# Kernel tuning notes

Measured on AMD Instinct MI355X. Metric: run time of the kernel, lower is better.

Reference implementation:

```python
import jax, jax.numpy as jnp
import numpy as np

N0, N1, N2 = 100000, 50000, 25000
E0, E1 = 400000, 200000
H1, D1 = 4, 64   # layer0: 4 heads x 64
H2, D2 = 1, 64   # layer1: 1 head  x 64
SLOPE = 0.2      # DGL GATConv leaky_relu negative_slope


def gat_conv(h_src, h_dst, src, dst, W, attn_l, attn_r, bias, n_dst, heads, d):
    # linear projection (shared between src and dst, as in DGL GATConv)
    f_src = (h_src @ W).reshape(-1, heads, d)   # (N_src, H, D)
    f_dst = (h_dst @ W).reshape(-1, heads, d)   # (N_dst, H, D)
    el = jnp.einsum('nhd,hd->nh', f_src, attn_l)  # (N_src, H)
    er = jnp.einsum('nhd,hd->nh', f_dst, attn_r)  # (N_dst, H)
    e = jax.nn.leaky_relu(el[src] + er[dst], SLOPE)  # (E, H)
    # edge-softmax over incoming edges of each dst node (numerically stable)
    m = jax.ops.segment_max(e, dst, num_segments=n_dst)      # (N_dst, H)
    ee = jnp.exp(e - m[dst])
    s = jax.ops.segment_sum(ee, dst, num_segments=n_dst)
    alpha = ee / s[dst]                                      # (E, H)
    msg = f_src[src] * alpha[:, :, None]                     # (E, H, D)
    out = jax.ops.segment_sum(msg, dst, num_segments=n_dst)  # (N_dst, H, D)
    return out + bias.reshape(1, heads, d)


def setup_inputs() -> dict:
    key = jax.random.key(0)
    ks = jax.random.split(key, 12)
    return {
        'x': jax.random.normal(ks[0], (N0, 256), jnp.float32),
        'e0_src': jax.random.randint(ks[1], (E0,), 0, N0, jnp.int32),
        'e0_dst': jax.random.randint(ks[2], (E0,), 0, N1, jnp.int32),
        'e1_src': jax.random.randint(ks[3], (E1,), 0, N1, jnp.int32),
        'e1_dst': jax.random.randint(ks[4], (E1,), 0, N2, jnp.int32),
        'W1': jax.random.normal(ks[5], (256, H1 * D1), jnp.float32) * 0.06,
        'al1': jax.random.normal(ks[6], (H1, D1), jnp.float32) * 0.1,
        'ar1': jax.random.normal(ks[7], (H1, D1), jnp.float32) * 0.1,
        'b1': jnp.zeros((H1 * D1,), jnp.float32),
        'W2': jax.random.normal(ks[8], (H1 * D1, H2 * D2), jnp.float32) * 0.06,
        'al2': jax.random.normal(ks[9], (H2, D2), jnp.float32) * 0.1,
        'ar2': jax.random.normal(ks[10], (H2, D2), jnp.float32) * 0.1,
        'b2': jnp.zeros((H2 * D2,), jnp.float32),
    }


def reference(x, e0_src, e0_dst, e1_src, e1_dst,
              W1, al1, ar1, b1, W2, al2, ar2, b2):
    # layer 0: block 100k src -> 50k dst; dst nodes are a prefix of src nodes
    h = gat_conv(x, x[:N1], e0_src, e0_dst, W1, al1, ar1, b1, N1, H1, D1)
    h = jax.nn.relu(h).reshape(N1, H1 * D1)   # activation + flatten(1); dropout is identity at eval
    # layer 1 (final): single head, no activation, flatten
    h = gat_conv(h, h[:N2], e1_src, e1_dst, W2, al2, ar2, b2, N2, H2, D2)
    return h.reshape(N2, H2 * D2)
```

## Files before the change

kernel.cpp:

```cpp
#include <hip/hip_runtime.h>
#include <cstddef>
#include <cstdint>

constexpr int cN0 = 100000, cN1 = 50000, cN2 = 25000;
constexpr int cE0 = 400000, cE1 = 200000;
constexpr float SLOPE = 0.2f;

typedef short short8  __attribute__((ext_vector_type(8)));
typedef float f32x4   __attribute__((ext_vector_type(4)));

__device__ __forceinline__ unsigned short f2bf(float x) {
    union { float f; uint32_t u; } c; c.f = x;
    uint32_t u = c.u + 0x7FFFu + ((c.u >> 16) & 1u);
    return (unsigned short)(u >> 16);
}
__device__ __forceinline__ float bf2f(uint32_t u) {
    union { uint32_t u; float f; } c; c.u = u << 16; return c.f;
}
__device__ __forceinline__ float lrelu(float x) { return x >= 0.f ? x : SLOPE * x; }

__device__ __forceinline__ uint32_t cvtpk(float lo, float hi) {
    uint32_t r;
    asm("v_cvt_pk_bf16_f32 %0, %1, %2" : "=v"(r) : "v"(lo), "v"(hi));
    return r;
}

__device__ __forceinline__ void gload_lds16(const void* g, void* l) {
    __builtin_amdgcn_global_load_lds(
        (const __attribute__((address_space(1))) unsigned int*)g,
        (__attribute__((address_space(3))) unsigned int*)l, 16, 0, 0);
}


__global__ void hist2_kernel(const int* __restrict__ d0, const int* __restrict__ d1,
                             int* __restrict__ cnt0, int* __restrict__ cnt1) {
    int i = blockIdx.x * blockDim.x + threadIdx.x;
    if (i < cE0) atomicAdd(&cnt0[d0[i]], 1);
    int j = i - cE0;
    if (j >= 0 && j < cE1) atomicAdd(&cnt1[d1[j]], 1);
}

__global__ __launch_bounds__(256) void chunk_sum2_kernel(const int* __restrict__ cnt0, int n0,
                                                         const int* __restrict__ cnt1, int n1,
                                                         int* __restrict__ bsum0, int* __restrict__ bsum1,
                                                         int nblk1) {
    const int* cnt = blockIdx.y ? cnt1 : cnt0;
    int n = blockIdx.y ? n1 : n0;
    int* bsum = blockIdx.y ? bsum1 : bsum0;
    if (blockIdx.y && (int)blockIdx.x >= nblk1) return;
    int i = blockIdx.x * 256 + threadIdx.x;
    int v = (i < n) ? cnt[i] : 0;
    #pragma unroll
    for (int o = 32; o; o >>= 1) v += __shfl_xor(v, o);
    __shared__ int ws[4];
    if ((threadIdx.x & 63) == 0) ws[threadIdx.x >> 6] = v;
    __syncthreads();
    if (threadIdx.x == 0) bsum[blockIdx.x] = ws[0] + ws[1] + ws[2] + ws[3];
}

__device__ __forceinline__ int block_exscan(int v, int& total) {
    int lane = threadIdx.x & 63, w = threadIdx.x >> 6;
    int x = v;
    #pragma unroll
    for (int o = 1; o < 64; o <<= 1) { int t = __shfl_up(x, o); if (lane >= o) x += t; }
    __shared__ int ws[4];
    if (lane == 63) ws[w] = x;
    __syncthreads();
    int add = 0;
    #pragma unroll
    for (int i = 0; i < 4; ++i) if (i < w) add += ws[i];
    total = ws[0] + ws[1] + ws[2] + ws[3];
    return add + x - v;
}

__global__ __launch_bounds__(256) void top_scan2_kernel(const int* __restrict__ bsum0, int nblk0,
                                                        const int* __restrict__ bsum1, int nblk1,
                                                        int* __restrict__ boff0, int* __restrict__ boff1,
                                                        int* __restrict__ tot0, int* __restrict__ tot1) {
    int i = threadIdx.x;
    int tot;
    int v = (i < nblk0) ? bsum0[i] : 0;
    int e = block_exscan(v, tot);
    if (i < nblk0) boff0[i] = e;
    if (i == 0) *tot0 = tot;
    __syncthreads();
    v = (i < nblk1) ? bsum1[i] : 0;
    e = block_exscan(v, tot);
    if (i < nblk1) boff1[i] = e;
    if (i == 0) *tot1 = tot;
}

__global__ __launch_bounds__(256) void chunk_scan2_kernel(const int* __restrict__ cnt0, int n0,
                                                          const int* __restrict__ cnt1, int n1,
                                                          const int* __restrict__ boff0, const int* __restrict__ boff1,
                                                          int* __restrict__ offs0, int* __restrict__ cursor0,
                                                          int* __restrict__ offs1, int* __restrict__ cursor1,
                                                          int nblk1) {
    const int* cnt = blockIdx.y ? cnt1 : cnt0;
    const int* boff = blockIdx.y ? boff1 : boff0;
    int* offs = blockIdx.y ? offs1 : offs0;
    int* cursor = blockIdx.y ? cursor1 : cursor0;
    int n = blockIdx.y ? n1 : n0;
    if (blockIdx.y && (int)blockIdx.x >= nblk1) return;
    int i = blockIdx.x * 256 + threadIdx.x;
    int v = (i < n) ? cnt[i] : 0;
    int tot; int e = block_exscan(v, tot) + boff[blockIdx.x];
    if (i < n) { offs[i] = e; cursor[i] = e; }
}

__global__ void scatter2_kernel(const int* __restrict__ s0, const int* __restrict__ d0,
                                const int* __restrict__ s1, const int* __restrict__ d1,
                                int* __restrict__ cursor0, int* __restrict__ srcidx0,
                                int* __restrict__ cursor1, int* __restrict__ srcidx1) {
    int i = blockIdx.x * blockDim.x + threadIdx.x;
    if (i < cE0) { int p = atomicAdd(&cursor0[d0[i]], 1); srcidx0[p] = s0[i]; }
    int j = i - cE0;
    if (j >= 0 && j < cE1) { int p = atomicAdd(&cursor1[d1[j]], 1); srcidx1[p] = s1[j]; }
}

__global__ __launch_bounds__(256) void bf16_transpose2_kernel(const float* __restrict__ W1,
                                                              const float* __restrict__ W2,
                                                              short* __restrict__ bt1,
                                                              short* __restrict__ bt2) {
    int i = blockIdx.x * 256 + threadIdx.x;
    if (i < 256 * 256) {
        int k = i >> 8, n = i & 255;
        bt1[(size_t)n * 256 + k] = (short)f2bf(W1[i]);
    } else {
        int j = i - 256 * 256;
        if (j < 256 * 64) {
            int k = j >> 6, n = j & 63;
            bt2[(size_t)n * 256 + k] = (short)f2bf(W2[j]);
        }
    }
}

__global__ __launch_bounds__(512, 4) void gemm0_deep(
    const float* __restrict__ A, const short* __restrict__ BT,
    unsigned short* __restrict__ C,
    const float* __restrict__ al, const float* __restrict__ ar,
    float* __restrict__ el, float* __restrict__ er,
    int M, int erN)
{
    constexpr int T = 8;
    constexpr int nh = 4;
    __shared__ float Asm[2][128 * 32];
    __shared__ short Bsm[2][256 * 32];

    const int tid = threadIdx.x;
    const int w = tid >> 6;
    const int lane = tid & 63;
    const int ln = lane & 15;
    const int kg = lane >> 4;
    const int wr = w >> 2;
    const int wc = w & 3;
    const int m0 = blockIdx.x * 128;

    f32x4 acc[4][4];
    #pragma unroll
    for (int mi = 0; mi < 4; ++mi)
        #pragma unroll
        for (int ni = 0; ni < 4; ++ni)
            #pragma unroll
            for (int j = 0; j < 4; ++j) acc[mi][ni][j] = 0.f;

    auto stageA = [&](int k0, int b) {
        #pragma unroll
        for (int q = 0; q < 2; ++q) {
            int ci = w + q * 8;
            int r = ci * 8 + (lane >> 3);
            int cl = (lane & 7) ^ (r & 7);
            int gr = m0 + r; if (gr >= M) gr = M - 1;
            gload_lds16(&A[(size_t)gr * 256 + k0 + cl * 4], &Asm[b][ci * 256]);
        }
    };
    auto stageB = [&](int k0, int b) {
        #pragma unroll
        for (int q = 0; q < 2; ++q) {
            int ci = w + q * 8;
            int r = ci * 16 + (lane >> 2);
            int cl = (lane & 3) ^ ((r >> 1) & 3);
            gload_lds16(&BT[(size_t)r * 256 + k0 + cl * 8], &Bsm[b][ci * 512]);
        }
    };

    stageA(0, 0); stageB(0, 0);
    __syncthreads();

    const int swa = ln & 7;
    const int p0base = 2 * kg;
    const int pb = kg ^ ((ln >> 1) & 3);

    int cur = 0;
    #pragma unroll
    for (int t = 0; t < T; ++t) {
        if (t + 1 < T) { stageA((t + 1) * 32, cur ^ 1); stageB((t + 1) * 32, cur ^ 1); }

        short8 af[4];
        {
            int pA = p0base ^ swa;
            #pragma unroll
            for (int mi = 0; mi < 4; ++mi) {
                int r = wr * 64 + mi * 16 + ln;
                const f32x4 q0 = *(const f32x4*)&Asm[cur][r * 32 + pA * 4];
                const f32x4 q1 = *(const f32x4*)&Asm[cur][r * 32 + (pA ^ 1) * 4];
                union { uint32_t u[4]; short8 s; } cv;
                cv.u[0] = cvtpk(q0[0], q0[1]);
                cv.u[1] = cvtpk(q0[2], q0[3]);
                cv.u[2] = cvtpk(q1[0], q1[1]);
                cv.u[3] = cvtpk(q1[2], q1[3]);
                af[mi] = cv.s;
            }
        }
        #pragma unroll
        for (int ni = 0; ni < 4; ++ni) {
            int rB = wc * 64 + ni * 16 + ln;
            short8 bf = *(const short8*)&Bsm[cur][rB * 32 + pb * 8];
            #pragma unroll
            for (int mi = 0; mi < 4; ++mi)
                acc[mi][ni] = __builtin_amdgcn_mfma_f32_16x16x32_bf16(af[mi], bf, acc[mi][ni], 0, 0, 0);
        }
        __syncthreads();
        cur ^= 1;
    }

    const int h = wc;
    float alv[4], arv[4];
    #pragma unroll
    for (int ni = 0; ni < 4; ++ni) {
        alv[ni] = al[h * 64 + ni * 16 + ln];
        arv[ni] = ar[h * 64 + ni * 16 + ln];
    }
    #pragma unroll
    for (int mi = 0; mi < 4; ++mi) {
        float pl[4] = {0, 0, 0, 0}, pr[4] = {0, 0, 0, 0};
        #pragma unroll
        for (int ni = 0; ni < 4; ++ni)
            #pragma unroll
            for (int j = 0; j < 4; ++j) {
                float v = acc[mi][ni][j];
                pl[j] += v * alv[ni];
                pr[j] += v * arv[ni];
            }
        #pragma unroll
        for (int j = 0; j < 4; ++j)
            #pragma unroll
            for (int o = 1; o < 16; o <<= 1) {
                pl[j] += __shfl_xor(pl[j], o);
                pr[j] += __shfl_xor(pr[j], o);
            }
        #pragma unroll
        for (int j = 0; j < 4; ++j) {
            int row = m0 + wr * 64 + mi * 16 + kg * 4 + j;
            if (row < M) {
                #pragma unroll
                for (int ni = 0; ni < 4; ++ni)
                    C[(size_t)row * 256 + wc * 64 + ni * 16 + ln] = f2bf(acc[mi][ni][j]);
                if (ln == 0) {
                    el[row * nh + h] = pl[j];
                    if (row < erN) er[row * nh + h] = pr[j];
                }
            }
        }
    }
}

__global__ __launch_bounds__(1024) void agg0_fused(
    const int* __restrict__ offs, const int* __restrict__ srcidx,
    const float* __restrict__ el, const float* __restrict__ er,
    const unsigned short* __restrict__ fb, const float* __restrict__ bias,
    const short* __restrict__ bt2,
    const float* __restrict__ al2, const float* __restrict__ ar2,
    unsigned short* __restrict__ f2b, float* __restrict__ el2, float* __restrict__ er2)
{
    constexpr int PITCH = 264;
    __shared__ short Bs2[64 * 256];
    __shared__ short h1s[16 * PITCH];
    __shared__ float partE[4][16];
    __shared__ float partR[4][16];

    const int tid = threadIdx.x;
    const int w = tid >> 6;
    const int lane = tid & 63;
    const int n = blockIdx.x * 16 + w;

    #pragma unroll
    for (int i = 0; i < 2; ++i) {
        int seg = 2 * (i * 16 + w);
        int r = seg + (lane >> 5);
        int c = (lane & 31) ^ (r & 7);
        gload_lds16(&bt2[(size_t)r * 256 + c * 8], &Bs2[(size_t)seg * 256]);
    }

    int beg = offs[n], end = offs[n + 1];

    int h4 = lane & 3, sub = lane >> 2;
    float erA = er[n * 4 + h4];
    float m = -1e30f, s = 0.f;
    for (int i = beg + sub; i < end; i += 16) {
        int sv = srcidx[i];
        float e = lrelu(el[sv * 4 + h4] + erA);
        if (e > m) { s = s * __expf(m - e) + 1.f; m = e; }
        else s += __expf(e - m);
    }
    #pragma unroll
    for (int o = 4; o < 64; o <<= 1) {
        float m2 = __shfl_xor(m, o), s2 = __shfl_xor(s, o);
        float M = fmaxf(m, m2);
        s = s * __expf(m - M) + s2 * __expf(m2 - M);
        m = M;
    }
    float inv = (s > 0.f) ? 1.f / s : 0.f;

    int q = lane >> 4, lcol = lane & 15;
    int hB = lcol >> 2;
    float mB = __shfl(m, hB);
    float invB = __shfl(inv, hB);
    float erB = __shfl(erA, hB);

    float a[16] = {};
    for (int i = beg + q; i < end; i += 4) {
        int sv = srcidx[i];
        float e = lrelu(el[sv * 4 + hB] + erB);
        float p = __expf(e - mB) * invB;
        const uint4* rp = (const uint4*)&fb[(size_t)sv * 256 + lcol * 16];
        uint4 v0 = rp[0];
        uint4 v1 = rp[1];
        a[0]  = fmaf(bf2f(v0.x & 0xffffu), p, a[0]);
        a[1]  = fmaf(bf2f(v0.x >> 16),     p, a[1]);
        a[2]  = fmaf(bf2f(v0.y & 0xffffu), p, a[2]);
        a[3]  = fmaf(bf2f(v0.y >> 16),     p, a[3]);
        a[4]  = fmaf(bf2f(v0.z & 0xffffu), p, a[4]);
        a[5]  = fmaf(bf2f(v0.z >> 16),     p, a[5]);
        a[6]  = fmaf(bf2f(v0.w & 0xffffu), p, a[6]);
        a[7]  = fmaf(bf2f(v0.w >> 16),     p, a[7]);
        a[8]  = fmaf(bf2f(v1.x & 0xffffu), p, a[8]);
        a[9]  = fmaf(bf2f(v1.x >> 16),     p, a[9]);
        a[10] = fmaf(bf2f(v1.y & 0xffffu), p, a[10]);
        a[11] = fmaf(bf2f(v1.y >> 16),     p, a[11]);
        a[12] = fmaf(bf2f(v1.z & 0xffffu), p, a[12]);
        a[13] = fmaf(bf2f(v1.z >> 16),     p, a[13]);
        a[14] = fmaf(bf2f(v1.w & 0xffffu), p, a[14]);
        a[15] = fmaf(bf2f(v1.w >> 16),     p, a[15]);
    }
    #pragma unroll
    for (int j = 0; j < 16; ++j) {
        a[j] += __shfl_xor(a[j], 16);
        a[j] += __shfl_xor(a[j], 32);
    }

    if (lane < 16) {
        float4 b0 = *(const float4*)&bias[lane * 16 + 0];
        float4 b1 = *(const float4*)&bias[lane * 16 + 4];
        float4 b2 = *(const float4*)&bias[lane * 16 + 8];
        float4 b3 = *(const float4*)&bias[lane * 16 + 12];
        float bb[16] = { b0.x, b0.y, b0.z, b0.w, b1.x, b1.y, b1.z, b1.w,
                         b2.x, b2.y, b2.z, b2.w, b3.x, b3.y, b3.z, b3.w };
        short8 r0, r1;
        #pragma unroll
        for (int j = 0; j < 8; ++j) {
            float o = a[j] + bb[j];
            r0[j] = (short)f2bf(o > 0.f ? o : 0.f);
        }
        #pragma unroll
        for (int j = 0; j < 8; ++j) {
            float o = a[8 + j] + bb[8 + j];
            r1[j] = (short)f2bf(o > 0.f ? o : 0.f);
        }
        *(short8*)&h1s[w * PITCH + lane * 16] = r0;
        *(short8*)&h1s[w * PITCH + lane * 16 + 8] = r1;
    }
    __syncthreads();

    if (w < 4) {
        const int ln = lane & 15, kg = lane >> 4;
        const int cc = w * 16 + ln;
        f32x4 acc2;
        #pragma unroll
        for (int j = 0; j < 4; ++j) acc2[j] = 0.f;
        #pragma unroll
        for (int kt = 0; kt < 8; ++kt) {
            short8 af = *(const short8*)&h1s[ln * PITCH + kt * 32 + kg * 8];
            short8 bf = *(const short8*)&Bs2[cc * 256 + ((kt * 4 + kg) ^ (cc & 7)) * 8];
            acc2 = __builtin_amdgcn_mfma_f32_16x16x32_bf16(af, bf, acc2, 0, 0, 0);
        }
        float alc = al2[cc], arc = ar2[cc];
        #pragma unroll
        for (int j = 0; j < 4; ++j) {
            int node = kg * 4 + j;
            float v = acc2[j];
            f2b[((size_t)(blockIdx.x * 16 + node)) * 64 + cc] = f2bf(v);
            float pe = v * alc, pr = v * arc;
            #pragma unroll
            for (int o = 1; o < 16; o <<= 1) {
                pe += __shfl_xor(pe, o);
                pr += __shfl_xor(pr, o);
            }
            if (ln == 0) { partE[w][node] = pe; partR[w][node] = pr; }
        }
    }
    __syncthreads();
    if (tid < 16) {
        int gn = blockIdx.x * 16 + tid;
        float e = partE[0][tid] + partE[1][tid] + partE[2][tid] + partE[3][tid];
        el2[gn] = e;
        if (gn < cN2) {
            float r = partR[0][tid] + partR[1][tid] + partR[2][tid] + partR[3][tid];
            er2[gn] = r;
        }
    }
}

__global__ __launch_bounds__(256) void agg1_kernel(const int* __restrict__ offs,
                                                   const int* __restrict__ srcidx,
                                                   const float* __restrict__ el,
                                                   const float* __restrict__ er,
                                                   const unsigned short* __restrict__ f2b,
                                                   const float* __restrict__ bias,
                                                   float* __restrict__ out) {
    int w = threadIdx.x >> 6, lane = threadIdx.x & 63;
    int n = blockIdx.x * 4 + w;
    if (n >= cN2) return;
    int beg = offs[n], end = offs[n + 1];
    float ern = er[n];

    float m = -1e30f, s = 0.f;
    for (int i = beg + lane; i < end; i += 64) {
        float e = lrelu(el[srcidx[i]] + ern);
        if (e > m) { s = s * __expf(m - e) + 1.f; m = e; }
        else s += __expf(e - m);
    }
    #pragma unroll
    for (int o = 1; o < 64; o <<= 1) {
        float m2 = __shfl_xor(m, o), s2 = __shfl_xor(s, o);
        float M = fmaxf(m, m2);
        s = s * __expf(m - M) + s2 * __expf(m2 - M);
        m = M;
    }
    float inv = (s > 0.f) ? 1.f / s : 0.f;

    int q = lane >> 3, lcol = lane & 7;
    float a[8] = {};
    for (int i = beg + q; i < end; i += 8) {
        int sv = srcidx[i];
        float e = lrelu(el[sv] + ern);
        float p = __expf(e - m) * inv;
        uint4 v = *(const uint4*)&f2b[(size_t)sv * 64 + lcol * 8];
        a[0] = fmaf(bf2f(v.x & 0xffffu), p, a[0]);
        a[1] = fmaf(bf2f(v.x >> 16),     p, a[1]);
        a[2] = fmaf(bf2f(v.y & 0xffffu), p, a[2]);
        a[3] = fmaf(bf2f(v.y >> 16),     p, a[3]);
        a[4] = fmaf(bf2f(v.z & 0xffffu), p, a[4]);
        a[5] = fmaf(bf2f(v.z >> 16),     p, a[5]);
        a[6] = fmaf(bf2f(v.w & 0xffffu), p, a[6]);
        a[7] = fmaf(bf2f(v.w >> 16),     p, a[7]);
    }
    #pragma unroll
    for (int j = 0; j < 8; ++j) {
        a[j] += __shfl_xor(a[j], 8);
        a[j] += __shfl_xor(a[j], 16);
        a[j] += __shfl_xor(a[j], 32);
    }
    if (q == 0) {
        float4 o0, o1;
        o0.x = a[0] + bias[lcol * 8 + 0];
        o0.y = a[1] + bias[lcol * 8 + 1];
        o0.z = a[2] + bias[lcol * 8 + 2];
        o0.w = a[3] + bias[lcol * 8 + 3];
        o1.x = a[4] + bias[lcol * 8 + 4];
        o1.y = a[5] + bias[lcol * 8 + 5];
        o1.z = a[6] + bias[lcol * 8 + 6];
        o1.w = a[7] + bias[lcol * 8 + 7];
        *(float4*)&out[(size_t)n * 64 + lcol * 8] = o0;
        *(float4*)&out[(size_t)n * 64 + lcol * 8 + 4] = o1;
    }
}


extern "C" void kernel_launch(void* const* d_in, const int* in_sizes, int n_in,
                              void* d_out, int out_size, void* d_ws, size_t ws_size,
                              hipStream_t stream) {
    const float* x      = (const float*)d_in[0];
    const int*   e0_src = (const int*)d_in[1];
    const int*   e0_dst = (const int*)d_in[2];
    const int*   e1_src = (const int*)d_in[3];
    const int*   e1_dst = (const int*)d_in[4];
    const float* W1     = (const float*)d_in[5];
    const float* al1    = (const float*)d_in[6];
    const float* ar1    = (const float*)d_in[7];
    const float* b1     = (const float*)d_in[8];
    const float* W2     = (const float*)d_in[9];
    const float* al2    = (const float*)d_in[10];
    const float* ar2    = (const float*)d_in[11];
    const float* b2     = (const float*)d_in[12];
    float* out = (float*)d_out;

    char* ws = (char*)d_ws;
    size_t off = 0;
    auto alloc = [&](size_t bytes) -> void* {
        void* p = ws + off;
        off = (off + bytes + 255) & ~(size_t)255;
        return p;
    };
    unsigned short* fb  = (unsigned short*)alloc((size_t)cN0 * 256 * 2);
    unsigned short* f2b = (unsigned short*)alloc((size_t)cN1 * 64 * 2);
    float* el0  = (float*)alloc((size_t)cN0 * 4 * 4);
    float* er0  = (float*)alloc((size_t)cN1 * 4 * 4);
    float* el2  = (float*)alloc((size_t)cN1 * 4);
    float* er2  = (float*)alloc((size_t)cN2 * 4);
    short* bt1  = (short*)alloc((size_t)256 * 256 * 2);
    short* bt2  = (short*)alloc((size_t)64 * 256 * 2);
    int* cntB    = (int*)alloc((size_t)(cN1 + cN2) * 4);
    int* cnt0    = cntB;
    int* cnt1    = cntB + cN1;
    int* offs0   = (int*)alloc((size_t)(cN1 + 1) * 4);
    int* cursor0 = (int*)alloc((size_t)cN1 * 4);
    int* srcidx0 = (int*)alloc((size_t)cE0 * 4);
    int* offs1   = (int*)alloc((size_t)(cN2 + 1) * 4);
    int* cursor1 = (int*)alloc((size_t)cN2 * 4);
    int* srcidx1 = (int*)alloc((size_t)cE1 * 4);
    int* bsum0   = (int*)alloc(256 * 4);
    int* boff0   = (int*)alloc(256 * 4);
    int* bsum1   = (int*)alloc(256 * 4);
    int* boff1   = (int*)alloc(256 * 4);
    (void)ws_size; (void)n_in; (void)in_sizes; (void)out_size;

    const int nblk0 = (cN1 + 255) / 256;
    const int nblk1 = (cN2 + 255) / 256;

    hipMemsetAsync(cntB, 0, (size_t)(cN1 + cN2) * 4, stream);
    hist2_kernel<<<(cE0 + cE1 + 255) / 256, 256, 0, stream>>>(e0_dst, e1_dst, cnt0, cnt1);
    chunk_sum2_kernel<<<dim3(nblk0, 2), 256, 0, stream>>>(cnt0, cN1, cnt1, cN2, bsum0, bsum1, nblk1);
    top_scan2_kernel<<<1, 256, 0, stream>>>(bsum0, nblk0, bsum1, nblk1, boff0, boff1,
                                            offs0 + cN1, offs1 + cN2);
    chunk_scan2_kernel<<<dim3(nblk0, 2), 256, 0, stream>>>(cnt0, cN1, cnt1, cN2, boff0, boff1,
                                                           offs0, cursor0, offs1, cursor1, nblk1);
    scatter2_kernel<<<(cE0 + cE1 + 255) / 256, 256, 0, stream>>>(e0_src, e0_dst, e1_src, e1_dst,
                                                                 cursor0, srcidx0, cursor1, srcidx1);
    bf16_transpose2_kernel<<<(256 * 256 + 256 * 64 + 255) / 256, 256, 0, stream>>>(W1, W2, bt1, bt2);

    gemm0_deep<<<(cN0 + 127) / 128, 512, 0, stream>>>(x, bt1, fb, al1, ar1, el0, er0, cN0, cN1);

    agg0_fused<<<cN1 / 16, 1024, 0, stream>>>(offs0, srcidx0, el0, er0, fb, b1,
                                              bt2, al2, ar2, f2b, el2, er2);

    agg1_kernel<<<(cN2 + 3) / 4, 256, 0, stream>>>(offs1, srcidx1, el2, er2, f2b, b2, out);
}
```

Measured before the change: 188.2 us.

## Replace 16-node MFMA fused layer-1 projection with per-wave scalar dot products

Shrinks the layer-0 aggregation kernel from 1024-thread blocks handling 16 nodes to 256-thread blocks handling 4 nodes. Each wave now computes its own node's 64-wide layer-1 projection with scalar bf16 FMAs, reading W2 rows straight from global memory instead of staging them in LDS and using MFMA. This removes the large LDS footprint and both block-wide barriers, which should raise occupancy and cut sync cost. In exchange, every wave re-reads the full 32KB W2 matrix through the cache hierarchy and does the projection on plain ALUs rather than matrix cores.

```diff
diff --git a/kernel.cpp b/kernel.cpp
--- a/kernel.cpp
+++ b/kernel.cpp
@@ -265,7 +265,7 @@
     }
 }
 
-__global__ __launch_bounds__(1024) void agg0_fused(
+__global__ __launch_bounds__(256) void agg0_kernel(
     const int* __restrict__ offs, const int* __restrict__ srcidx,
     const float* __restrict__ el, const float* __restrict__ er,
     const unsigned short* __restrict__ fb, const float* __restrict__ bias,
@@ -273,25 +273,11 @@
     const float* __restrict__ al2, const float* __restrict__ ar2,
     unsigned short* __restrict__ f2b, float* __restrict__ el2, float* __restrict__ er2)
 {
-    constexpr int PITCH = 264;
-    __shared__ short Bs2[64 * 256];
-    __shared__ short h1s[16 * PITCH];
-    __shared__ float partE[4][16];
-    __shared__ float partR[4][16];
-
-    const int tid = threadIdx.x;
-    const int w = tid >> 6;
-    const int lane = tid & 63;
-    const int n = blockIdx.x * 16 + w;
-
-    #pragma unroll
-    for (int i = 0; i < 2; ++i) {
-        int seg = 2 * (i * 16 + w);
-        int r = seg + (lane >> 5);
-        int c = (lane & 31) ^ (r & 7);
-        gload_lds16(&bt2[(size_t)r * 256 + c * 8], &Bs2[(size_t)seg * 256]);
-    }
-
+    __shared__ short h1s[4][256];
+
+    int w = threadIdx.x >> 6, lane = threadIdx.x & 63;
+    int n = blockIdx.x * 4 + w;
+    if (n >= cN1) return;
     int beg = offs[n], end = offs[n + 1];
 
     int h4 = lane & 3, sub = lane >> 2;
@@ -349,65 +335,44 @@
         a[j] += __shfl_xor(a[j], 32);
     }
 
-    if (lane < 16) {
-        float4 b0 = *(const float4*)&bias[lane * 16 + 0];
-        float4 b1 = *(const float4*)&bias[lane * 16 + 4];
-        float4 b2 = *(const float4*)&bias[lane * 16 + 8];
-        float4 b3 = *(const float4*)&bias[lane * 16 + 12];
-        float bb[16] = { b0.x, b0.y, b0.z, b0.w, b1.x, b1.y, b1.z, b1.w,
-                         b2.x, b2.y, b2.z, b2.w, b3.x, b3.y, b3.z, b3.w };
+    if (q == 0) {
         short8 r0, r1;
         #pragma unroll
         for (int j = 0; j < 8; ++j) {
-            float o = a[j] + bb[j];
+            float o = a[j] + bias[lcol * 16 + j];
             r0[j] = (short)f2bf(o > 0.f ? o : 0.f);
         }
         #pragma unroll
         for (int j = 0; j < 8; ++j) {
-            float o = a[8 + j] + bb[8 + j];
+            float o = a[8 + j] + bias[lcol * 16 + 8 + j];
             r1[j] = (short)f2bf(o > 0.f ? o : 0.f);
         }
-        *(short8*)&h1s[w * PITCH + lane * 16] = r0;
-        *(short8*)&h1s[w * PITCH + lane * 16 + 8] = r1;
-    }
-    __syncthreads();
-
-    if (w < 4) {
-        const int ln = lane & 15, kg = lane >> 4;
-        const int cc = w * 16 + ln;
-        f32x4 acc2;
-        #pragma unroll
-        for (int j = 0; j < 4; ++j) acc2[j] = 0.f;
-        #pragma unroll
-        for (int kt = 0; kt < 8; ++kt) {
-            short8 af = *(const short8*)&h1s[ln * PITCH + kt * 32 + kg * 8];
-            short8 bf = *(const short8*)&Bs2[cc * 256 + ((kt * 4 + kg) ^ (cc & 7)) * 8];
-            acc2 = __builtin_amdgcn_mfma_f32_16x16x32_bf16(af, bf, acc2, 0, 0, 0);
-        }
-        float alc = al2[cc], arc = ar2[cc];
-        #pragma unroll
-        for (int j = 0; j < 4; ++j) {
-            int node = kg * 4 + j;
-            float v = acc2[j];
-            f2b[((size_t)(blockIdx.x * 16 + node)) * 64 + cc] = f2bf(v);
-            float pe = v * alc, pr = v * arc;
-            #pragma unroll
-            for (int o = 1; o < 16; o <<= 1) {
-                pe += __shfl_xor(pe, o);
-                pr += __shfl_xor(pr, o);
-            }
-            if (ln == 0) { partE[w][node] = pe; partR[w][node] = pr; }
-        }
-    }
-    __syncthreads();
-    if (tid < 16) {
-        int gn = blockIdx.x * 16 + tid;
-        float e = partE[0][tid] + partE[1][tid] + partE[2][tid] + partE[3][tid];
-        el2[gn] = e;
-        if (gn < cN2) {
-            float r = partR[0][tid] + partR[1][tid] + partR[2][tid] + partR[3][tid];
-            er2[gn] = r;
-        }
+        *(short8*)&h1s[w][lcol * 16] = r0;
+        *(short8*)&h1s[w][lcol * 16 + 8] = r1;
+    }
+
+    float acc2 = 0.f;
+    const short* wrow = &bt2[(size_t)lane * 256];
+    #pragma unroll 8
+    for (int kt = 0; kt < 32; ++kt) {
+        short8 hv = *(const short8*)&h1s[w][kt * 8];
+        short8 wv = *(const short8*)&wrow[kt * 8];
+        #pragma unroll
+        for (int j = 0; j < 8; ++j)
+            acc2 = fmaf(bf2f((uint32_t)(unsigned short)hv[j]),
+                        bf2f((uint32_t)(unsigned short)wv[j]), acc2);
+    }
+    f2b[(size_t)n * 64 + lane] = f2bf(acc2);
+    float pe = acc2 * al2[lane];
+    float pr = acc2 * ar2[lane];
+    #pragma unroll
+    for (int o = 1; o < 64; o <<= 1) {
+        pe += __shfl_xor(pe, o);
+        pr += __shfl_xor(pr, o);
+    }
+    if (lane == 0) {
+        el2[n] = pe;
+        if (n < cN2) er2[n] = pr;
     }
 }
 
@@ -541,8 +506,8 @@
 
     gemm0_deep<<<(cN0 + 127) / 128, 512, 0, stream>>>(x, bt1, fb, al1, ar1, el0, er0, cN0, cN1);
 
-    agg0_fused<<<cN1 / 16, 1024, 0, stream>>>(offs0, srcidx0, el0, er0, fb, b1,
-                                              bt2, al2, ar2, f2b, el2, er2);
+    agg0_kernel<<<(cN1 + 3) / 4, 256, 0, stream>>>(offs0, srcidx0, el0, er0, fb, b1,
+                                                   bt2, al2, ar2, f2b, el2, er2);
 
     agg1_kernel<<<(cN2 + 3) / 4, 256, 0, stream>>>(offs1, srcidx1, el2, er2, f2b, b2, out);
 }
```

Measured after the change: 339.2 us. 1.8x slower.
